# Kernel optimization log

Hardware: AMD Instinct MI355X
Metric: run time of the kernel (lower is better)

Reference implementation:

```python
import jax, jax.numpy as jnp
import numpy as np

B, S, D, UNITS = 8, 2048, 512, 512

def setup_inputs() -> dict:
    key = jax.random.key(0)
    k1, k2, k3, k4 = jax.random.split(key, 4)
    scale = 1.0 / np.sqrt(D)
    return {
        "x": jax.random.normal(k1, (B, S, D), dtype=jnp.float32),
        "Wq": jax.random.normal(k2, (D, UNITS), dtype=jnp.float32) * scale,
        "Wk": jax.random.normal(k3, (D, UNITS), dtype=jnp.float32) * scale,
        "Wv": jax.random.normal(k4, (D, UNITS), dtype=jnp.float32) * scale,
    }

def reference(x, Wq, Wk, Wv):
    # Q, K, V: [B, S, units]
    Q = jnp.einsum('bsd,du->bsu', x, Wq)
    Km = jnp.einsum('bsd,du->bsu', x, Wk)
    V = jnp.einsum('bsd,du->bsu', x, Wv)
    d_k = jnp.asarray(Wq.shape[-1], dtype=x.dtype)
    # scores: [B, S, S]
    scores = jnp.einsum('bqu,bku->bqk', Q, Km) / jnp.sqrt(d_k)
    attn = jax.nn.softmax(scores, axis=-1)
    return jnp.einsum('bqk,bku->bqu', attn, V)
```

## Files before the change

### kernel.cpp

```cpp
#include <hip/hip_runtime.h>

typedef __attribute__((ext_vector_type(8))) __bf16 bf16x8;
typedef __attribute__((ext_vector_type(4))) float f32x4;
typedef unsigned short u16;
typedef unsigned int u32;

#define VMCNT(n) asm volatile("s_waitcnt vmcnt(" #n ")" ::: "memory")
#define LGKMCNT0 asm volatile("s_waitcnt lgkmcnt(0)" ::: "memory")

__device__ __forceinline__ u16 f2bf(float f) {
  union { float f; u32 u; } v; v.f = f;
  u32 r = v.u + 0x7FFFu + ((v.u >> 16) & 1u);
  return (u16)(r >> 16);
}
__device__ __forceinline__ float fexp2(float x) {
  float r; asm("v_exp_f32 %0, %1" : "=v"(r) : "v"(x)); return r;
}

__global__ __launch_bounds__(256) void cast_x_kernel(const float* __restrict__ x,
                                                     u16* __restrict__ xb, int n4) {
  int i = blockIdx.x * 256 + threadIdx.x;
  if (i >= n4) return;
  float4 v = reinterpret_cast<const float4*>(x)[i];
  ushort4 o;
  o.x = f2bf(v.x); o.y = f2bf(v.y); o.z = f2bf(v.z); o.w = f2bf(v.w);
  reinterpret_cast<ushort4*>(xb)[i] = o;
}

__global__ __launch_bounds__(1024) void transpose_w_kernel(const float* __restrict__ Wq,
                                                           const float* __restrict__ Wk,
                                                           const float* __restrict__ Wv,
                                                           u16* __restrict__ Wt) {
  const float* src = blockIdx.z == 0 ? Wq : (blockIdx.z == 1 ? Wk : Wv);
  u16* dst = Wt + (size_t)blockIdx.z * 512 * 512;
  __shared__ float tile[32][33];
  int u0 = blockIdx.x * 32, d0 = blockIdx.y * 32;
  tile[threadIdx.y][threadIdx.x] = src[(d0 + threadIdx.y) * 512 + u0 + threadIdx.x];
  __syncthreads();
  dst[(u0 + threadIdx.y) * 512 + d0 + threadIdx.x] = f2bf(tile[threadIdx.x][threadIdx.y]);
}

__global__ __launch_bounds__(256) void qkv_kernel(const u16* __restrict__ Xb,
                                                  const u16* __restrict__ Wt3,
                                                  u16* __restrict__ Q, u16* __restrict__ K,
                                                  u16* __restrict__ Vt2) {
  __shared__ u16 As[3][128 * 32], Bs[3][128 * 32];
  const int bm = blockIdx.y * 128;
  const int bn = blockIdx.x * 128;
  const int z = blockIdx.z;
  const u16* A = Xb + (size_t)bm * 512;
  const u16* Bt = Wt3 + (size_t)z * 512 * 512 + (size_t)bn * 512;

  const int t = threadIdx.x;
  const int lane = t & 63;
  const int w = t >> 6;
  const int wr = w >> 1, wc = w & 1;
  const int la = lane & 15;
  const int q = lane >> 4;
  f32x4 acc[4][4] = {};

  auto stage = [&](int buf, int kt) {
    const int k0 = kt * 32;
#pragma unroll
    for (int it = 0; it < 2; ++it) {
      int c = it * 256 + t, row = c >> 2;
      int col = ((c & 3) ^ ((row >> 1) & 3)) << 3;
      __builtin_amdgcn_global_load_lds(
          (const __attribute__((address_space(1))) void*)(A + (size_t)row * 512 + k0 + col),
          (__attribute__((address_space(3))) void*)(&As[buf][c * 8]), 16, 0, 0);
    }
#pragma unroll
    for (int it = 0; it < 2; ++it) {
      int c = it * 256 + t, row = c >> 2;
      int col = ((c & 3) ^ ((row >> 1) & 3)) << 3;
      __builtin_amdgcn_global_load_lds(
          (const __attribute__((address_space(1))) void*)(Bt + (size_t)row * 512 + k0 + col),
          (__attribute__((address_space(3))) void*)(&Bs[buf][c * 8]), 16, 0, 0);
    }
  };

  auto body = [&](int buf) {
    bf16x8 a[4], b[4];
#pragma unroll
    for (int i = 0; i < 4; ++i) {
      int row = wr * 64 + i * 16 + la;
      a[i] = *reinterpret_cast<const bf16x8*>(&As[buf][row * 32 + ((q ^ ((row >> 1) & 3)) << 3)]);
    }
#pragma unroll
    for (int j = 0; j < 4; ++j) {
      int row = wc * 64 + j * 16 + la;
      b[j] = *reinterpret_cast<const bf16x8*>(&Bs[buf][row * 32 + ((q ^ ((row >> 1) & 3)) << 3)]);
    }
    __builtin_amdgcn_s_setprio(1);
#pragma unroll
    for (int i = 0; i < 4; ++i)
#pragma unroll
      for (int j = 0; j < 4; ++j)
        acc[i][j] = __builtin_amdgcn_mfma_f32_16x16x32_bf16(a[i], b[j], acc[i][j], 0, 0, 0);
    __builtin_amdgcn_s_setprio(0);
  };

  stage(0, 0); stage(1, 1);
  int cb = 0, sb = 2;
  for (int kt = 0; kt < 14; ++kt) {
    VMCNT(4);
    __builtin_amdgcn_s_barrier();
    stage(sb, kt + 2);
    body(cb);
    cb = (cb == 2) ? 0 : cb + 1;
    sb = (sb == 2) ? 0 : sb + 1;
  }
  VMCNT(4); __builtin_amdgcn_s_barrier(); body(2);
  VMCNT(0); __builtin_amdgcn_s_barrier(); body(0);

  const int r0 = q * 4, cn = lane & 15;
  if (z < 2) {
    u16* out = (z == 0) ? Q : K;
#pragma unroll
    for (int i = 0; i < 4; ++i)
#pragma unroll
      for (int j = 0; j < 4; ++j)
#pragma unroll
        for (int r = 0; r < 4; ++r) {
          int m = bm + 64 * wr + 16 * i + r0 + r;
          int n = bn + 64 * wc + 16 * j + cn;
          out[(size_t)m * 512 + n] = f2bf(acc[i][j][r]);
        }
  } else {
#pragma unroll
    for (int i = 0; i < 4; ++i)
#pragma unroll
      for (int j = 0; j < 4; ++j)
#pragma unroll
        for (int r = 0; r < 4; ++r) {
          int m = bm + 64 * wr + 16 * i + r0 + r;
          int u = bn + 64 * wc + 16 * j + cn;
          int b = m >> 11, s = m & 2047;
          Vt2[(((size_t)b * 64 + (s >> 5)) * 512 + u) * 32 + (s & 31)] = f2bf(acc[i][j][r]);
        }
  }
}

__global__ __launch_bounds__(1024, 4) void scores_kernel(const u16* __restrict__ Q,
                                                         const u16* __restrict__ K,
                                                         u16* __restrict__ S2) {
  __shared__ u16 ring[3][2][256 * 32];
  const int bb = blockIdx.x;
  const int bm = blockIdx.y * 256;
  const int bn = blockIdx.z * 256;
  const u16* Aq = Q + (size_t)(bb * 2048 + bm) * 512;
  const u16* Bk = K + (size_t)(bb * 2048 + bn) * 512;

  const int t = threadIdx.x;
  const int lane = t & 63;
  const int wid = t >> 6;
  const int wm = wid >> 2;
  const int wn = wid & 3;
  const int la = lane & 15;
  const int q = lane >> 4;

  f32x4 acc[4][4] = {};

  auto stage = [&](int kt) {
    const int buf = kt % 3;
    const int koff = kt * 32;
    {
      int c = t, row = c >> 2;
      int col = ((c & 3) ^ ((row >> 1) & 3)) << 3;
      __builtin_amdgcn_global_load_lds(
          (const __attribute__((address_space(1))) void*)(Aq + (size_t)row * 512 + koff + col),
          (__attribute__((address_space(3))) void*)(&ring[buf][0][c * 8]), 16, 0, 0);
      __builtin_amdgcn_global_load_lds(
          (const __attribute__((address_space(1))) void*)(Bk + (size_t)row * 512 + koff + col),
          (__attribute__((address_space(3))) void*)(&ring[buf][1][c * 8]), 16, 0, 0);
    }
  };

  auto body = [&](int kt) {
    const int buf = kt % 3;
    const u16* At = ring[buf][0];
    const u16* Bt = ring[buf][1];
    bf16x8 a[4], b[4];
#pragma unroll
    for (int i = 0; i < 4; ++i) {
      int row = wm * 64 + i * 16 + la;
      a[i] = *reinterpret_cast<const bf16x8*>(At + row * 32 + ((q ^ ((row >> 1) & 3)) << 3));
    }
#pragma unroll
    for (int j = 0; j < 4; ++j) {
      int row = wn * 64 + j * 16 + la;
      b[j] = *reinterpret_cast<const bf16x8*>(Bt + row * 32 + ((q ^ ((row >> 1) & 3)) << 3));
    }
    __builtin_amdgcn_s_setprio(1);
#pragma unroll
    for (int i = 0; i < 4; ++i)
#pragma unroll
      for (int j = 0; j < 4; ++j)
        acc[i][j] = __builtin_amdgcn_mfma_f32_16x16x32_bf16(a[i], b[j], acc[i][j], 0, 0, 0);
    __builtin_amdgcn_s_setprio(0);
  };

  stage(0); stage(1);
  for (int kt = 0; kt < 14; ++kt) {
    VMCNT(2);
    __builtin_amdgcn_s_barrier();
    stage(kt + 2);
    body(kt);
  }
  VMCNT(2); __builtin_amdgcn_s_barrier(); body(14);
  VMCNT(0); __builtin_amdgcn_s_barrier(); body(15);

  const float scale = 0.06375872127f;
  const int r0h = q * 4;
#pragma unroll
  for (int i = 0; i < 4; ++i)
#pragma unroll
    for (int j = 0; j < 4; ++j) {
      int n = bn + wn * 64 + j * 16;
      int kt_j = n >> 5;
      int ke_j = (n & 31) + la;
      u16* dst = S2 + ((size_t)(bb * 64 + kt_j) * 2048) * 32 + ke_j;
#pragma unroll
      for (int r = 0; r < 4; ++r) {
        int m = bm + wm * 64 + i * 16 + r0h + r;
        dst[(size_t)m * 32] = f2bf(fexp2(acc[i][j][r] * scale));
      }
    }
}

__global__ __launch_bounds__(512, 4) void pv_kernel(const u16* __restrict__ S2,
                                                    const u16* __restrict__ Vt2,
                                                    float* __restrict__ out) {
  __shared__ __align__(16) char smem[65536];
  __shared__ float larr2[2][128];
  u16* As = (u16*)smem;
  u16* Bs = As + 2 * 8192;
  float* scratch = (float*)smem;

  const int id = blockIdx.x;
  const int b = id & 7;
  const int local = id >> 3;
  const int bn = (local & 3) * 128;
  const int bm = (local >> 2) * 128;

  const u16* A2 = S2 + ((size_t)b * 64 * 2048 + (size_t)bm) * 32;
  const u16* B2 = Vt2 + ((size_t)b * 64 * 512 + (size_t)bn) * 32;

  const int t = threadIdx.x;
  const int lane = t & 63;
  const int wid = t >> 6;
  const int wm = (wid >> 2) & 1;
  const int wn = (wid >> 1) & 1;
  const int wk = wid & 1;
  const int la = lane & 15;
  const int q = lane >> 4;

  f32x4 acc[4][4] = {};
  float lacc[4] = {0.f, 0.f, 0.f, 0.f};

  auto stage = [&](int s) {
    const int buf = s & 1;
#pragma unroll
    for (int it = 0; it < 2; ++it) {
      int c = it * 512 + t;
      int row = c >> 3, pslot = c & 7;
      int lslot = pslot ^ (row & 7);
      __builtin_amdgcn_global_load_lds(
          (const __attribute__((address_space(1))) void*)(
              A2 + (size_t)(2 * s + (lslot >> 2)) * 65536 + row * 32 + (lslot & 3) * 8),
          (__attribute__((address_space(3))) void*)(As + buf * 8192 + c * 8), 16, 0, 0);
    }
#pragma unroll
    for (int it = 0; it < 2; ++it) {
      int c = it * 512 + t;
      int row = c >> 3, pslot = c & 7;
      int lslot = pslot ^ (row & 7);
      __builtin_amdgcn_global_load_lds(
          (const __attribute__((address_space(1))) void*)(
              B2 + (size_t)(2 * s + (lslot >> 2)) * 16384 + row * 32 + (lslot & 3) * 8),
          (__attribute__((address_space(3))) void*)(Bs + buf * 8192 + c * 8), 16, 0, 0);
    }
  };

  bf16x8 a[4], bb[4];
  auto rd = [&](int buf) {
    const u16* Ab = As + buf * 8192;
    const u16* Bb = Bs + buf * 8192;
#pragma unroll
    for (int i = 0; i < 4; ++i) {
      int row = wm * 64 + i * 16 + la;
      int ps = (wk * 4 + q) ^ (row & 7);
      a[i] = *reinterpret_cast<const bf16x8*>(Ab + row * 64 + ps * 8);
    }
#pragma unroll
    for (int j = 0; j < 4; ++j) {
      int row = wn * 64 + j * 16 + la;
      int ps = (wk * 4 + q) ^ (row & 7);
      bb[j] = *reinterpret_cast<const bf16x8*>(Bb + row * 64 + ps * 8);
    }
  };
  auto compute = [&]() {
    if (wn == 0) {
#pragma unroll
      for (int i = 0; i < 4; ++i) {
        float ls = 0.f;
#pragma unroll
        for (int e = 0; e < 8; ++e) ls += (float)a[i][e];
        lacc[i] += ls;
      }
    }
    __builtin_amdgcn_s_setprio(1);
#pragma unroll
    for (int i = 0; i < 4; ++i)
#pragma unroll
      for (int j = 0; j < 4; ++j)
        acc[i][j] = __builtin_amdgcn_mfma_f32_16x16x32_bf16(a[i], bb[j], acc[i][j], 0, 0, 0);
    __builtin_amdgcn_s_setprio(0);
  };

  stage(0); stage(1);
  for (int s = 0; s < 30; ++s) {
    VMCNT(4);
    __builtin_amdgcn_s_barrier();
    rd(s & 1);
    LGKMCNT0;
    __builtin_amdgcn_s_barrier();
    stage(s + 2);
    compute();
  }
  VMCNT(4); __builtin_amdgcn_s_barrier();
  rd(0); LGKMCNT0; __builtin_amdgcn_s_barrier(); compute();
  VMCNT(0); __builtin_amdgcn_s_barrier();
  rd(1); LGKMCNT0; __builtin_amdgcn_s_barrier();
  compute();

  float l[4];
#pragma unroll
  for (int i = 0; i < 4; ++i) {
    l[i] = lacc[i];
    l[i] += __shfl_xor(l[i], 16);
    l[i] += __shfl_xor(l[i], 32);
  }
  if (wn == 0 && q == 0) {
#pragma unroll
    for (int i = 0; i < 4; ++i) larr2[wk][wm * 64 + i * 16 + la] = l[i];
  }
  float* sp = scratch + (wid >> 1) * 4096;
  if (wk == 1) {
#pragma unroll
    for (int i = 0; i < 4; ++i)
#pragma unroll
      for (int j = 0; j < 4; ++j)
        *reinterpret_cast<f32x4*>(sp + (i * 4 + j) * 256 + lane * 4) = acc[i][j];
  }
  __syncthreads();
  if (wk == 0) {
#pragma unroll
    for (int i = 0; i < 4; ++i)
#pragma unroll
      for (int j = 0; j < 4; ++j) {
        f32x4 o = *reinterpret_cast<const f32x4*>(sp + (i * 4 + j) * 256 + lane * 4);
#pragma unroll
        for (int r = 0; r < 4; ++r) acc[i][j][r] += o[r];
      }
    float* C = out + ((size_t)b * 2048 + bm) * 512;
    const int r0 = q * 4, cn = lane & 15;
    float inv[4][4];
#pragma unroll
    for (int i = 0; i < 4; ++i)
#pragma unroll
      for (int r = 0; r < 4; ++r) {
        int row = wm * 64 + i * 16 + r0 + r;
        inv[i][r] = 1.0f / (larr2[0][row] + larr2[1][row]);
      }
#pragma unroll
    for (int i = 0; i < 4; ++i)
#pragma unroll
      for (int j = 0; j < 4; ++j)
#pragma unroll
        for (int r = 0; r < 4; ++r) {
          int m = wm * 64 + 16 * i + r0 + r;
          int n = bn + 64 * wn + 16 * j + cn;
          C[(size_t)m * 512 + n] = acc[i][j][r] * inv[i][r];
        }
  }
}

extern "C" void kernel_launch(void* const* d_in, const int* in_sizes, int n_in,
                              void* d_out, int out_size, void* d_ws, size_t ws_size,
                              hipStream_t stream) {
  const float* x  = (const float*)d_in[0];
  const float* Wq = (const float*)d_in[1];
  const float* Wk = (const float*)d_in[2];
  const float* Wv = (const float*)d_in[3];
  float* out = (float*)d_out;

  char* p = (char*)d_ws;
  u16* Xb = (u16*)p;            p += (size_t)16384 * 512 * 2;
  u16* Wt = (u16*)p;            p += (size_t)3 * 512 * 512 * 2;
  u16* Q  = (u16*)p;            p += (size_t)16384 * 512 * 2;
  u16* K  = (u16*)p;            p += (size_t)16384 * 512 * 2;
  u16* Vt2 = (u16*)p;           p += (size_t)16384 * 512 * 2;
  u16* S2 = (u16*)p;

  cast_x_kernel<<<dim3(8192), dim3(256), 0, stream>>>(x, Xb, 16384 * 512 / 4);
  transpose_w_kernel<<<dim3(16, 16, 3), dim3(32, 32), 0, stream>>>(Wq, Wk, Wv, Wt);
  qkv_kernel<<<dim3(4, 128, 3), dim3(256), 0, stream>>>(Xb, Wt, Q, K, Vt2);
  scores_kernel<<<dim3(8, 8, 8), dim3(1024), 0, stream>>>(Q, K, S2);
  pv_kernel<<<dim3(512), dim3(512), 0, stream>>>(S2, Vt2, out);
}
```

Baseline: 138.2 us.

## Fuse Q/K/V projections into one wide-N tile per X row block

The QKV projection kernel now treats the three weight matrices as one concatenated 1536-wide N dimension. Each 1024-thread block computes a 128x384 tile, with 16 waves arranged 2x8 and each wave covering 64x48. The aim is to load each X tile once for more output columns, cutting redundant A-tile global traffic and launching fewer, larger blocks. In exchange, shared memory per block grows, each wave holds fewer accumulators, and the epilogue picks Q, K or V per column, which may add branching.

```diff
diff --git a/kernel.cpp b/kernel.cpp
--- a/kernel.cpp
+++ b/kernel.cpp
@@ -40,105 +40,100 @@
   dst[(u0 + threadIdx.y) * 512 + d0 + threadIdx.x] = f2bf(tile[threadIdx.x][threadIdx.y]);
 }
 
-__global__ __launch_bounds__(256) void qkv_kernel(const u16* __restrict__ Xb,
-                                                  const u16* __restrict__ Wt3,
-                                                  u16* __restrict__ Q, u16* __restrict__ K,
-                                                  u16* __restrict__ Vt2) {
-  __shared__ u16 As[3][128 * 32], Bs[3][128 * 32];
+__global__ __launch_bounds__(1024, 4) void qkv_kernel(const u16* __restrict__ Xb,
+                                                      const u16* __restrict__ Wt3,
+                                                      u16* __restrict__ Q, u16* __restrict__ K,
+                                                      u16* __restrict__ Vt2) {
+  __shared__ u16 As[3][128 * 32], Bs[3][384 * 32];
+  const int nt = blockIdx.x;
   const int bm = blockIdx.y * 128;
-  const int bn = blockIdx.x * 128;
-  const int z = blockIdx.z;
   const u16* A = Xb + (size_t)bm * 512;
-  const u16* Bt = Wt3 + (size_t)z * 512 * 512 + (size_t)bn * 512;
+  const u16* Bt = Wt3 + (size_t)nt * 384 * 512;
 
   const int t = threadIdx.x;
   const int lane = t & 63;
-  const int w = t >> 6;
-  const int wr = w >> 1, wc = w & 1;
+  const int wid = t >> 6;
+  const int wm = wid >> 3;
+  const int wn = wid & 7;
   const int la = lane & 15;
   const int q = lane >> 4;
-  f32x4 acc[4][4] = {};
-
-  auto stage = [&](int buf, int kt) {
+  f32x4 acc[4][3] = {};
+
+  auto stage = [&](int kt) {
+    const int buf = kt % 3;
     const int k0 = kt * 32;
 #pragma unroll
     for (int it = 0; it < 2; ++it) {
-      int c = it * 256 + t, row = c >> 2;
-      int col = ((c & 3) ^ ((row >> 1) & 3)) << 3;
-      __builtin_amdgcn_global_load_lds(
-          (const __attribute__((address_space(1))) void*)(A + (size_t)row * 512 + k0 + col),
-          (__attribute__((address_space(3))) void*)(&As[buf][c * 8]), 16, 0, 0);
-    }
-#pragma unroll
-    for (int it = 0; it < 2; ++it) {
-      int c = it * 256 + t, row = c >> 2;
-      int col = ((c & 3) ^ ((row >> 1) & 3)) << 3;
-      __builtin_amdgcn_global_load_lds(
-          (const __attribute__((address_space(1))) void*)(Bt + (size_t)row * 512 + k0 + col),
-          (__attribute__((address_space(3))) void*)(&Bs[buf][c * 8]), 16, 0, 0);
-    }
-  };
-
-  auto body = [&](int buf) {
-    bf16x8 a[4], b[4];
+      int cid = it * 1024 + t;
+      if (cid < 512) {
+        int a = cid, row = a >> 2;
+        int col = ((a & 3) ^ ((row >> 1) & 3)) << 3;
+        __builtin_amdgcn_global_load_lds(
+            (const __attribute__((address_space(1))) void*)(A + (size_t)row * 512 + k0 + col),
+            (__attribute__((address_space(3))) void*)(&As[buf][a * 8]), 16, 0, 0);
+      } else {
+        int e = cid - 512, row = e >> 2;
+        int col = ((e & 3) ^ ((row >> 1) & 3)) << 3;
+        __builtin_amdgcn_global_load_lds(
+            (const __attribute__((address_space(1))) void*)(Bt + (size_t)row * 512 + k0 + col),
+            (__attribute__((address_space(3))) void*)(&Bs[buf][e * 8]), 16, 0, 0);
+      }
+    }
+  };
+
+  auto body = [&](int kt) {
+    const int buf = kt % 3;
+    bf16x8 a[4], b[3];
 #pragma unroll
     for (int i = 0; i < 4; ++i) {
-      int row = wr * 64 + i * 16 + la;
+      int row = wm * 64 + i * 16 + la;
       a[i] = *reinterpret_cast<const bf16x8*>(&As[buf][row * 32 + ((q ^ ((row >> 1) & 3)) << 3)]);
     }
 #pragma unroll
-    for (int j = 0; j < 4; ++j) {
-      int row = wc * 64 + j * 16 + la;
+    for (int j = 0; j < 3; ++j) {
+      int row = wn * 48 + j * 16 + la;
       b[j] = *reinterpret_cast<const bf16x8*>(&Bs[buf][row * 32 + ((q ^ ((row >> 1) & 3)) << 3)]);
     }
     __builtin_amdgcn_s_setprio(1);
 #pragma unroll
     for (int i = 0; i < 4; ++i)
 #pragma unroll
-      for (int j = 0; j < 4; ++j)
+      for (int j = 0; j < 3; ++j)
         acc[i][j] = __builtin_amdgcn_mfma_f32_16x16x32_bf16(a[i], b[j], acc[i][j], 0, 0, 0);
     __builtin_amdgcn_s_setprio(0);
   };
 
-  stage(0, 0); stage(1, 1);
-  int cb = 0, sb = 2;
+  stage(0); stage(1);
   for (int kt = 0; kt < 14; ++kt) {
-    VMCNT(4);
+    VMCNT(2);
     __builtin_amdgcn_s_barrier();
-    stage(sb, kt + 2);
-    body(cb);
-    cb = (cb == 2) ? 0 : cb + 1;
-    sb = (sb == 2) ? 0 : sb + 1;
-  }
-  VMCNT(4); __builtin_amdgcn_s_barrier(); body(2);
-  VMCNT(0); __builtin_amdgcn_s_barrier(); body(0);
+    stage(kt + 2);
+    body(kt);
+  }
+  VMCNT(2); __builtin_amdgcn_s_barrier(); body(14);
+  VMCNT(0); __builtin_amdgcn_s_barrier(); body(15);
 
   const int r0 = q * 4, cn = lane & 15;
-  if (z < 2) {
-    u16* out = (z == 0) ? Q : K;
-#pragma unroll
-    for (int i = 0; i < 4; ++i)
-#pragma unroll
-      for (int j = 0; j < 4; ++j)
-#pragma unroll
-        for (int r = 0; r < 4; ++r) {
-          int m = bm + 64 * wr + 16 * i + r0 + r;
-          int n = bn + 64 * wc + 16 * j + cn;
-          out[(size_t)m * 512 + n] = f2bf(acc[i][j][r]);
-        }
-  } else {
-#pragma unroll
-    for (int i = 0; i < 4; ++i)
-#pragma unroll
-      for (int j = 0; j < 4; ++j)
-#pragma unroll
-        for (int r = 0; r < 4; ++r) {
-          int m = bm + 64 * wr + 16 * i + r0 + r;
-          int u = bn + 64 * wc + 16 * j + cn;
+#pragma unroll
+  for (int i = 0; i < 4; ++i)
+#pragma unroll
+    for (int j = 0; j < 3; ++j) {
+      int col = nt * 384 + wn * 48 + j * 16 + cn;
+      int z = col >> 9;
+      int u = col & 511;
+#pragma unroll
+      for (int r = 0; r < 4; ++r) {
+        int m = bm + wm * 64 + i * 16 + r0 + r;
+        if (z == 0) {
+          Q[(size_t)m * 512 + u] = f2bf(acc[i][j][r]);
+        } else if (z == 1) {
+          K[(size_t)m * 512 + u] = f2bf(acc[i][j][r]);
+        } else {
           int b = m >> 11, s = m & 2047;
           Vt2[(((size_t)b * 64 + (s >> 5)) * 512 + u) * 32 + (s & 31)] = f2bf(acc[i][j][r]);
         }
-  }
+      }
+    }
 }
 
 __global__ __launch_bounds__(1024, 4) void scores_kernel(const u16* __restrict__ Q,
@@ -405,7 +400,7 @@
 
   cast_x_kernel<<<dim3(8192), dim3(256), 0, stream>>>(x, Xb, 16384 * 512 / 4);
   transpose_w_kernel<<<dim3(16, 16, 3), dim3(32, 32), 0, stream>>>(Wq, Wk, Wv, Wt);
-  qkv_kernel<<<dim3(4, 128, 3), dim3(256), 0, stream>>>(Xb, Wt, Q, K, Vt2);
+  qkv_kernel<<<dim3(4, 128), dim3(1024), 0, stream>>>(Xb, Wt, Q, K, Vt2);
   scores_kernel<<<dim3(8, 8, 8), dim3(1024), 0, stream>>>(Q, K, S2);
   pv_kernel<<<dim3(512), dim3(512), 0, stream>>>(S2, Vt2, out);
 }
```

After: 167.6 us. +21.2%, slower.
